# Performance work log

Measured on AMD Instinct MI355X. Metric: run time of the kernel, lower is better.

The kernel has to match this reference:

```python
import jax, jax.numpy as jnp
import numpy as np

R = 128; C = 64; S = 3; NL = 2; NH = 4; B = 2; V = 4; N = R * R
HD = C // NH
PLANES = ['xy', 'xz', 'yz']


def _sample_points(plane):
    lin = np.linspace(-1.0, 1.0, R, dtype=np.float32)
    gx, gy = np.meshgrid(lin, lin, indexing='xy')
    s = np.linspace(-1.0, 1.0, S, dtype=np.float32)
    gxs = np.broadcast_to(gx[..., None], (R, R, S))
    gys = np.broadcast_to(gy[..., None], (R, R, S))
    ss = np.broadcast_to(s[None, None, :], (R, R, S))
    if plane == 'xy':
        coords = np.stack([gxs, gys, ss], -1)
    elif plane == 'xz':
        coords = np.stack([gxs, ss, gys], -1)
    else:
        coords = np.stack([ss, gxs, gys], -1)
    return jnp.asarray(coords)  # [R,R,S,3]


def _layer_norm(x, g, b):
    m = jnp.mean(x, -1, keepdims=True)
    v = jnp.var(x, -1, keepdims=True)
    return (x - m) / jnp.sqrt(v + 1e-5) * g + b


def _grid_sample_border(feat, grid):
    # feat [Bb,Ch,H,W], grid [Bb,P,2] (treated as normalized coords, align_corners=True, border pad)
    H, W = feat.shape[2], feat.shape[3]
    gx = jnp.clip((grid[..., 0] + 1.0) * 0.5 * (W - 1), 0.0, W - 1)
    gy = jnp.clip((grid[..., 1] + 1.0) * 0.5 * (H - 1), 0.0, H - 1)
    x0 = jnp.floor(gx).astype(jnp.int32); y0 = jnp.floor(gy).astype(jnp.int32)
    x1 = jnp.minimum(x0 + 1, W - 1); y1 = jnp.minimum(y0 + 1, H - 1)
    wx = (gx - x0)[..., None]; wy = (gy - y0)[..., None]
    ft = feat.transpose(0, 2, 3, 1)  # [Bb,H,W,Ch]
    bi = jnp.arange(feat.shape[0])[:, None]
    v00 = ft[bi, y0, x0]; v01 = ft[bi, y0, x1]; v10 = ft[bi, y1, x0]; v11 = ft[bi, y1, x1]
    out = (1 - wy) * ((1 - wx) * v00 + wx * v01) + wy * ((1 - wx) * v10 + wx * v11)
    return out.transpose(0, 2, 1)  # [Bb,Ch,P]


def _splat(features, pts):
    # features [BV,C,Np], pts [BV,Np,3] in [-1,1] -> [BV,3,R,R,C]
    f = features.transpose(0, 2, 1)
    g = jnp.clip((pts + 1.0) * (R - 1) / 2.0, 0.0, R - 1 - 1e-5)
    x, y, z = g[..., 0], g[..., 1], g[..., 2]
    x0 = jnp.floor(x).astype(jnp.int32); y0 = jnp.floor(y).astype(jnp.int32); z0 = jnp.floor(z).astype(jnp.int32)
    wx = x - x0; wy = y - y0; wz = z - z0
    x1 = jnp.minimum(x0 + 1, R - 1); y1 = jnp.minimum(y0 + 1, R - 1); z1 = jnp.minimum(z0 + 1, R - 1)
    w000 = (1 - wx) * (1 - wy) * (1 - wz); w001 = (1 - wx) * (1 - wy) * wz
    w010 = (1 - wx) * wy * (1 - wz)
    w100 = wx * (1 - wy) * (1 - wz)
    w110 = wx * wy * (1 - wz); w111 = wx * wy * wz
    bv = features.shape[0]
    bi = jnp.arange(bv)[:, None]

    def plane_accum(pairs):
        tri = jnp.zeros((bv, R, R, C), features.dtype)
        wac = jnp.zeros((bv, R, R), features.dtype)
        for w, ia, ib in pairs:
            tri = tri.at[bi, ia, ib].add(w[..., None] * f)
            wac = wac.at[bi, ia, ib].add(w)
        return tri / jnp.maximum(wac, 1e-8)[..., None]

    # corner/weight pairings replicated exactly from the source (incl. its asymmetries)
    p0 = plane_accum([(w000, x0, y0), (w010, x0, y1), (w100, x1, y0), (w110, x1, y1)])
    p1 = plane_accum([(w000, x0, z0), (w001, x0, z1), (w100, x1, z0), (w111, x1, z1)])
    p2 = plane_accum([(w000, y0, z0), (w001, y0, z1), (w010, y1, z0), (w111, y1, z1)])
    return jnp.stack([p0, p1, p2], 1)


def _project(points, plane, plane_feats):
    sel = {'xy': (0, 1), 'xz': (0, 2), 'yz': (1, 2)}
    feats = []
    for i, op in enumerate(PLANES):
        if op == plane:
            continue
        a, bidx = sel[op]
        coords = jnp.stack([points[..., a], points[..., bidx]], -1)  # [R,R,S,2]
        # faithful to source: pixel coords are fed to grid_sample as if normalized
        gc = jnp.clip((coords * 0.5 + 0.5) * (R - 1), 0.0, R - 1)
        pf = plane_feats[i].reshape(B, R, R, C).transpose(0, 3, 1, 2)  # [B,C,H,W]
        grid = jnp.broadcast_to(gc.reshape(1, R * R * S, 2), (B, R * R * S, 2))
        samp = _grid_sample_border(pf, grid).reshape(B, C, R, R, S).transpose(0, 2, 3, 4, 1)
        feats.append(samp)
    return jnp.concatenate(feats, 3)  # [B,R,R,2S,C]


def _mha(x, ctx, in_w, in_b, ow, ob):
    # x [M,1,C], ctx [M,T,C]; torch MultiheadAttention (eval, no dropout)
    wq, wk, wv = in_w[:C], in_w[C:2 * C], in_w[2 * C:]
    bq, bk, bv = in_b[:C], in_b[C:2 * C], in_b[2 * C:]
    M, T = ctx.shape[0], ctx.shape[1]
    q = (x @ wq.T + bq).reshape(M, 1, NH, HD)
    k = (ctx @ wk.T + bk).reshape(M, T, NH, HD)
    v = (ctx @ wv.T + bv).reshape(M, T, NH, HD)
    att = jnp.einsum('mqhd,mthd->mhqt', q, k) * (1.0 / np.sqrt(HD))
    p = jax.nn.softmax(att, -1)
    o = jnp.einsum('mhqt,mthd->mqhd', p, v).reshape(M, 1, C)
    return o @ ow.T + ob


def _forward(img_feats, pts, query_tensors, ln1_g, ln1_b, ln2_g, ln2_b,
             in_w, in_b, out_w, out_b, ffn_w1, ffn_b1, ffn_w2, ffn_b2):
    bv = B * V
    tri = _splat(img_feats.reshape(bv, C, N), pts.reshape(bv, N, 3))  # [BV,3,R,R,C]
    tri = tri.reshape(B, V, 3, R, R, C).mean(1)  # aggregate views
    plane_feats = [tri[:, i].reshape(B, N, C) + query_tensors[i].reshape(1, N, C) for i in range(3)]
    sp = {p: _sample_points(p) for p in PLANES}
    T = 2 * S
    for l in range(NL):
        new = []
        for i, plane in enumerate(PLANES):
            ctx = _project(sp[plane], plane, plane_feats).reshape(B, N, T, C)
            x = plane_feats[i]
            xn = _layer_norm(x, ln1_g[l], ln1_b[l])
            cn = _layer_norm(ctx, ln1_g[l], ln1_b[l])
            M = B * N
            ao = _mha(xn.reshape(M, 1, C), cn.reshape(M, T, C),
                      in_w[l], in_b[l], out_w[l], out_b[l]).reshape(B, N, C)
            x = x + ao
            xn2 = _layer_norm(x, ln2_g[l], ln2_b[l])
            h = jax.nn.gelu(xn2 @ ffn_w1[l].T + ffn_b1[l], approximate=False) @ ffn_w2[l].T + ffn_b2[l]
            new.append(x + h)
        plane_feats = new
    out = jnp.stack([f.reshape(B, R, R, C) for f in plane_feats], 1)
    return out.transpose(0, 1, 4, 2, 3)  # [B,3,C,R,R]


def setup_inputs() -> dict:
    key = jax.random.key(0)
    ks = jax.random.split(key, 8)
    d = {}
    d['img_feats'] = jax.random.normal(ks[0], (B, V, C, N), jnp.float32)
    d['pts'] = jax.random.uniform(ks[1], (B, V, N, 3), jnp.float32, -1.0, 1.0)
    d['query_tensors'] = jax.random.normal(ks[2], (3, R, R, C), jnp.float32) * 0.02
    d['ln1_g'] = jnp.ones((NL, C), jnp.float32)
    d['ln1_b'] = jnp.zeros((NL, C), jnp.float32)
    d['ln2_g'] = jnp.ones((NL, C), jnp.float32)
    d['ln2_b'] = jnp.zeros((NL, C), jnp.float32)
    d['in_w'] = jax.random.normal(ks[3], (NL, 3 * C, C), jnp.float32) * 0.05
    d['in_b'] = jnp.zeros((NL, 3 * C), jnp.float32)
    d['out_w'] = jax.random.normal(ks[4], (NL, C, C), jnp.float32) * 0.05
    d['out_b'] = jnp.zeros((NL, C), jnp.float32)
    d['ffn_w1'] = jax.random.normal(ks[5], (NL, 4 * C, C), jnp.float32) * 0.05
    d['ffn_b1'] = jnp.zeros((NL, 4 * C), jnp.float32)
    d['ffn_w2'] = jax.random.normal(ks[6], (NL, C, 4 * C), jnp.float32) * 0.05
    d['ffn_b2'] = jnp.zeros((NL, C), jnp.float32)
    return d


def reference(img_feats, pts, query_tensors, ln1_g, ln1_b, ln2_g, ln2_b,
              in_w, in_b, out_w, out_b, ffn_w1, ffn_b1, ffn_w2, ffn_b2):
    return _forward(img_feats, pts, query_tensors, ln1_g, ln1_b, ln2_g, ln2_b,
                    in_w, in_b, out_w, out_b, ffn_w1, ffn_b1, ffn_w2, ffn_b2)
```

## Files before the change

### kernel.cpp

```cpp
#include <hip/hip_runtime.h>
#include <math.h>

constexpr int R_ = 128, C_ = 64, NL_ = 2, B_ = 2, V_ = 4;
constexpr int N_ = R_ * R_;
constexpr int T_ = 6;

typedef __attribute__((ext_vector_type(8))) short bf16x8;
typedef __attribute__((ext_vector_type(4))) float f32x4;
typedef __attribute__((ext_vector_type(4))) unsigned short u16x4;
typedef __attribute__((ext_vector_type(8))) unsigned short u16x8;

#define MFMA_B16(a, b, c) __builtin_amdgcn_mfma_f32_16x16x32_bf16((a), (b), (c), 0, 0, 0)

constexpr int OFF_O = 12288, OFF_W1 = 16384, OFF_W2 = 32768;
constexpr int PK_ELEMS = 49152;
constexpr int LAYER_PK = 2 * PK_ELEMS;

constexpr int NBV = B_ * V_;
constexpr size_t FTR_SZ = (size_t)NBV * N_ * C_;
constexpr int NSEG = 3 * NBV;
constexpr size_t SEG_SZ = (size_t)NSEG * N_;
constexpr int OSTRIDE = N_ + 128;
constexpr size_t KV_SZ = (size_t)3 * B_ * T_ * 128 * 64;

__device__ inline unsigned rne16(float x) {
    unsigned b = __float_as_uint(x);
    return (b + 0x7fffu + ((b >> 16) & 1u)) >> 16;
}

__device__ inline float wsum(float v) {
#pragma unroll
    for (int m = 1; m < 64; m <<= 1) v += __shfl_xor(v, m, 64);
    return v;
}

__device__ inline float lnorm(float v, float g, float b) {
    float m = wsum(v) * (1.f / 64.f);
    float d = v - m;
    float var = wsum(d * d) * (1.f / 64.f);
    return d * rsqrtf(var + 1e-5f) * g + b;
}

__device__ inline void stageW(const float* __restrict__ W, float* buf, int tid) {
#pragma unroll
    for (int it = 0; it < 4; ++it) {
        int idx4 = it * 256 + tid;
        int r = idx4 >> 4, u4 = idx4 & 15;
        float4 v = ((const float4*)W)[idx4];
        *(float4*)&buf[r * 68 + u4 * 4] = v;
    }
}

__device__ inline bf16x8 readFrag(const unsigned short* base, int rowBase, int lane,
                                  int ks, int rowStrideB, int swzMask) {
    int rowloc = rowBase + (lane & 15);
    int off = rowloc * rowStrideB + ks * 64 + ((lane >> 4) & 3) * 16;
    off ^= ((rowloc & swzMask) << 4);
    return *(const bf16x8*)((const char*)base + off);
}

__device__ inline void storeA4(unsigned short* base, int rloc, int cb,
                               float v0, float v1, float v2, float v3) {
    u16x4 u;
    u[0] = (unsigned short)rne16(v0);
    u[1] = (unsigned short)rne16(v1);
    u[2] = (unsigned short)rne16(v2);
    u[3] = (unsigned short)rne16(v3);
    int bo = (rloc * 128 + cb * 8) ^ ((rloc & 7) << 4);
    *(u16x4*)((char*)base + bo) = u;
}

__device__ inline void readB(const unsigned short* matHi, int E, int NTm, int ks, int nt,
                             int lane, bf16x8& bh, bf16x8& bl) {
    int off = (((ks * NTm + nt) << 6) + lane) << 3;
    bh = *(const bf16x8*)(matHi + off);
    bl = *(const bf16x8*)(matHi + E + off);
}

__global__ __launch_bounds__(256) void pack_layer(const float* __restrict__ iw,
                                                  const float* __restrict__ ow,
                                                  const float* __restrict__ w1,
                                                  const float* __restrict__ w2,
                                                  unsigned short* __restrict__ pk) {
    int idx = blockIdx.x * 256 + threadIdx.x;
    if (idx >= PK_ELEMS) return;
    const float* W;
    int O, K, base, mode, lidx;
    if (idx < 12288)      { int m = idx >> 12; lidx = idx & 4095; W = iw + m * 4096; O = 64;  K = 64;  base = m * 4096; mode = 0; }
    else if (idx < 16384) { lidx = idx - 12288; W = ow; O = 64;  K = 64;  base = OFF_O;  mode = 0; }
    else if (idx < 32768) { lidx = idx - 16384; W = w1; O = 256; K = 64;  base = OFF_W1; mode = 0; }
    else                  { lidx = idx - 32768; W = w2; O = 64;  K = 256; base = OFF_W2; mode = 1; }
    int j = lidx & 7, l = (lidx >> 3) & 63, rem = lidx >> 9;
    int NTm = O >> 4;
    int nt = rem & (NTm - 1), ks = rem / NTm;
    int kfrag = ks * 32 + ((l >> 4) & 3) * 8 + j;
    int k;
    if (mode == 0) { int p = kfrag & 63; k = (p & 3) * 16 + (p >> 2); }
    else { int cc = kfrag >> 7; int pl = kfrag & 127; k = (cc * 8 + (pl & 7)) * 16 + (pl >> 3); }
    int o = nt * 16 + (l & 15);
    float w = W[(size_t)o * K + k];
    unsigned hb = rne16(w);
    float hf = __uint_as_float(hb << 16);
    unsigned lb = rne16(w - hf);
    int E = O * K;
    pk[2 * base + lidx] = (unsigned short)hb;
    pk[2 * base + E + lidx] = (unsigned short)lb;
}

__global__ __launch_bounds__(256) void init_feats(const float* __restrict__ q,
                                                  float* __restrict__ f0) {
    int idx = blockIdx.x * 256 + threadIdx.x;
    if (idx >= 3 * N_ * C_) return;
    int p = idx / (N_ * C_);
    int rem = idx - p * (N_ * C_);
    float val = q[idx];
    f0[(size_t)(p * B_ + 0) * N_ * C_ + rem] = val;
    f0[(size_t)(p * B_ + 1) * N_ * C_ + rem] = val;
}

__global__ __launch_bounds__(256) void zero_counts(int4* __restrict__ p, int n4) {
    int i = blockIdx.x * 256 + threadIdx.x;
    if (i < n4) p[i] = make_int4(0, 0, 0, 0);
}

__global__ __launch_bounds__(256) void transpose_feats(const float* __restrict__ src,
                                                       float* __restrict__ dst) {
    __shared__ float tile[64][65];
    int blk = blockIdx.x;
    int ntile = blk & 255;
    int bv = blk >> 8;
    int n0 = ntile * 64;
    int tr = threadIdx.x >> 6, tc = threadIdx.x & 63;
    const float* s = src + (size_t)bv * C_ * N_;
#pragma unroll
    for (int it = 0; it < 16; ++it) {
        int c = it * 4 + tr;
        tile[c][tc] = s[(size_t)c * N_ + n0 + tc];
    }
    __syncthreads();
    float* d = dst + ((size_t)bv * N_ + n0) * C_;
#pragma unroll
    for (int it = 0; it < 16; ++it) {
        int r = it * 4 + tr;
        d[(size_t)r * C_ + tc] = tile[tc][r];
    }
}

__global__ __launch_bounds__(256) void bin_count(const float* __restrict__ pts,
                                                 int* __restrict__ counts) {
    int idx = blockIdx.x * 256 + threadIdx.x;
    if (idx >= NBV * N_) return;
    int bv = idx >> 14;
    const float* p = pts + (size_t)idx * 3;
    float px = p[0], py = p[1], pz = p[2];
    const float HI = (float)(127.0 - 1e-5);
    float gx = fminf(fmaxf((px + 1.0f) * 127.0f / 2.0f, 0.0f), HI);
    float gy = fminf(fmaxf((py + 1.0f) * 127.0f / 2.0f, 0.0f), HI);
    float gz = fminf(fmaxf((pz + 1.0f) * 127.0f / 2.0f, 0.0f), HI);
    int x0 = (int)gx, y0 = (int)gy, z0 = (int)gz;
    atomicAdd(&counts[(0 * NBV + bv) * N_ + x0 * R_ + y0], 1);
    atomicAdd(&counts[(1 * NBV + bv) * N_ + x0 * R_ + z0], 1);
    atomicAdd(&counts[(2 * NBV + bv) * N_ + y0 * R_ + z0], 1);
}

__global__ __launch_bounds__(256) void scan_bins(const int* __restrict__ counts,
                                                 int* __restrict__ offsets,
                                                 int* __restrict__ cursors) {
    __shared__ int part[256];
    int seg = blockIdx.x;
    int t = threadIdx.x;
    const int* c = counts + (size_t)seg * N_;
    int sum = 0;
    for (int i = 0; i < 64; ++i) sum += c[t * 64 + i];
    part[t] = sum;
    __syncthreads();
    if (t == 0) {
        int run = 0;
        for (int i = 0; i < 256; ++i) { int v = part[i]; part[i] = run; run += v; }
    }
    __syncthreads();
    int run = part[t];
    int* o = offsets + (size_t)seg * OSTRIDE;
    int* cu = cursors + (size_t)seg * N_;
    for (int i = 0; i < 64; ++i) {
        o[t * 64 + i] = run;
        cu[t * 64 + i] = run;
        run += c[t * 64 + i];
    }
    if (t < 128) o[N_ + t] = N_;
}

__global__ __launch_bounds__(256) void scatter_pts(const float* __restrict__ pts,
                                                   int* __restrict__ cursors,
                                                   float4* __restrict__ ent) {
    int idx = blockIdx.x * 256 + threadIdx.x;
    if (idx >= NBV * N_) return;
    int bv = idx >> 14, n = idx & (N_ - 1);
    const float* p = pts + (size_t)idx * 3;
    float px = p[0], py = p[1], pz = p[2];
    const float HI = (float)(127.0 - 1e-5);
    float gx = fminf(fmaxf((px + 1.0f) * 127.0f / 2.0f, 0.0f), HI);
    float gy = fminf(fmaxf((py + 1.0f) * 127.0f / 2.0f, 0.0f), HI);
    float gz = fminf(fmaxf((pz + 1.0f) * 127.0f / 2.0f, 0.0f), HI);
    int x0 = (int)gx, y0 = (int)gy, z0 = (int)gz;
    float4 e;
    e.x = __uint_as_float((unsigned)n);
    e.y = gx - (float)x0; e.z = gy - (float)y0; e.w = gz - (float)z0;
    int s0 = 0 * NBV + bv, s1 = 1 * NBV + bv, s2 = 2 * NBV + bv;
    int p0 = atomicAdd(&cursors[(size_t)s0 * N_ + x0 * R_ + y0], 1);
    ent[(size_t)s0 * N_ + p0] = e;
    int p1 = atomicAdd(&cursors[(size_t)s1 * N_ + x0 * R_ + z0], 1);
    ent[(size_t)s1 * N_ + p1] = e;
    int p2 = atomicAdd(&cursors[(size_t)s2 * N_ + y0 * R_ + z0], 1);
    ent[(size_t)s2 * N_ + p2] = e;
}

__global__ __launch_bounds__(512) void gather_splat(
    const float* __restrict__ ftr, const int* __restrict__ offsets,
    const float4* __restrict__ ent, float* __restrict__ f0) {
    __shared__ float sfacc[8][8][64];
    __shared__ float swsum[8][8];
    int wid = threadIdx.x >> 6, lane = threadIdx.x & 63;
    int v = wid >> 1, dr = wid & 1;
    int strip = blockIdx.x;
    int pi = blockIdx.y, b = blockIdx.z;
    int a = strip >> 4;
    int c0 = (strip & 15) << 3;

    int bv = b * V_ + v;
    int seg = pi * NBV + bv;
    const int* ob = offsets + (size_t)seg * OSTRIDE;
    const float4* eb = ent + (size_t)seg * N_;
    const float* fbase = ftr + (size_t)bv * N_ * C_ + lane;
    float facc[8], wsum_[8];
#pragma unroll
    for (int k = 0; k < 8; ++k) { facc[k] = 0.f; wsum_[k] = 0.f; }

    int ba = a - dr;
    if (ba >= 0) {
        int rowbase = ba * R_ + c0 - 1;
        int o[10];
#pragma unroll
        for (int jj = 0; jj < 10; ++jj)
            o[jj] = ob[max(rowbase + jj, 0)];
#pragma unroll
        for (int j = 0; j < 9; ++j) {
            if (j == 0 && c0 == 0) continue;
            int e = o[j + 1];
            for (int i = o[j]; i < e; ++i) {
                float4 r = eb[i];
                int n = (int)__float_as_uint(r.x);
                float wx = r.y, wy = r.z, wz = r.w;
                float ax = 1.f - wx, ay = 1.f - wy, az = 1.f - wz;
                float XA = dr ? wx : ax;
                float YA = dr ? wy : ay;
                float w0 = (pi == 2 ? ax * YA : XA * ay) * az;
                float w1 = (pi == 0) ? XA * wy * az : XA * YA * wz;
                float f = fbase[(size_t)n * C_];
                if (j > 0) { facc[j - 1] += w0 * f; wsum_[j - 1] += w0; }
                if (j < 8) { facc[j] += w1 * f; wsum_[j] += w1; }
            }
        }
    }
#pragma unroll
    for (int k = 0; k < 8; ++k) sfacc[wid][k][lane] = facc[k];
    if (lane == 0) {
#pragma unroll
        for (int k = 0; k < 8; ++k) swsum[wid][k] = wsum_[k];
    }
    __syncthreads();

    int k = wid;
    float tot = 0.f;
#pragma unroll
    for (int v2 = 0; v2 < 4; ++v2) {
        float fa = sfacc[v2 * 2][k][lane] + sfacc[v2 * 2 + 1][k][lane];
        float wsv = swsum[v2 * 2][k] + swsum[v2 * 2 + 1][k];
        tot += fa / fmaxf(wsv, 1e-8f);
    }
    float* dst = f0 + (((size_t)(pi * B_ + b)) * N_ + a * R_ + c0 + k) * C_ + lane;
    *dst += 0.25f * tot;
}

__global__ __launch_bounds__(256) void ctx_kv(
    const float* __restrict__ fin,
    const float* __restrict__ ln1g, const float* __restrict__ ln1b,
    const float* __restrict__ inw, const float* __restrict__ inb,
    float* __restrict__ kvk, float* __restrict__ kvv) {
    __shared__ float s_wk[64 * 68];
    __shared__ float s_wv[64 * 68];
    __shared__ float s_act[32 * 68];
    int tid = threadIdx.x, wid = tid >> 6, lane = tid & 63;
    stageW(inw + 4096, s_wk, tid);
    stageW(inw + 8192, s_wv, tid);

    int rid0 = blockIdx.x * 32 + wid * 8;
    int seg = rid0 >> 7;
    int pos0 = rid0 & 127;
    int t = seg % 6;
    int pib = seg / 6;
    int pi = pib >> 1, b = pib & 1;
    int khalf = (t < 3) ? t : t - 3;
    float sk = (float)(khalf - 1);
    bool tl = t < 3;
    int io;
    if (pi == 0) io = tl ? 1 : 2;
    else if (pi == 1) io = tl ? 0 : 2;
    else io = tl ? 0 : 1;
    const float* Fio = fin + (size_t)(io * B_ + b) * N_ * 64;
    float g1 = ln1g[lane], b1 = ln1b[lane];

#pragma unroll
    for (int rr = 0; rr < 8; ++rr) {
        int pos = pos0 + rr;
        float lp = -1.0f + (2.0f * (float)pos) / 127.0f;
        float caf, cbf;
        if (pi == 0) { caf = lp; cbf = sk; }
        else if (pi == 1) { if (tl) { caf = lp; cbf = sk; } else { caf = sk; cbf = lp; } }
        else { caf = sk; cbf = lp; }
        float ua = fminf(fmaxf((caf * 0.5f + 0.5f) * 127.0f, 0.0f), 127.0f);
        float ub = fminf(fmaxf((cbf * 0.5f + 0.5f) * 127.0f, 0.0f), 127.0f);
        float gxp = fminf(fmaxf(((ua + 1.0f) * 0.5f) * 127.0f, 0.0f), 127.0f);
        float gyp = fminf(fmaxf(((ub + 1.0f) * 0.5f) * 127.0f, 0.0f), 127.0f);
        int xx0 = (int)gxp, yy0 = (int)gyp;
        int xx1 = xx0 + 1 < 128 ? xx0 + 1 : 127;
        int yy1 = yy0 + 1 < 128 ? yy0 + 1 : 127;
        float wx = gxp - (float)xx0, wy = gyp - (float)yy0;
        float v00 = Fio[(size_t)(yy0 * R_ + xx0) * 64 + lane];
        float v01 = Fio[(size_t)(yy0 * R_ + xx1) * 64 + lane];
        float v10 = Fio[(size_t)(yy1 * R_ + xx0) * 64 + lane];
        float v11 = Fio[(size_t)(yy1 * R_ + xx1) * 64 + lane];
        float cv = (1.0f - wy) * ((1.0f - wx) * v00 + wx * v01) +
                   wy * ((1.0f - wx) * v10 + wx * v11);
        s_act[(wid * 8 + rr) * 68 + lane] = lnorm(cv, g1, b1);
    }
    __syncthreads();

    float kk[8], vv[8];
    float bk = inb[64 + lane], bv = inb[128 + lane];
#pragma unroll
    for (int rr = 0; rr < 8; ++rr) { kk[rr] = bk; vv[rr] = bv; }
    const float* wrk = s_wk + lane * 68;
    const float* wrv = s_wv + lane * 68;
#pragma unroll 4
    for (int g = 0; g < 16; ++g) {
        float4 wk4 = *(const float4*)(wrk + g * 4);
        float4 wv4 = *(const float4*)(wrv + g * 4);
#pragma unroll
        for (int rr = 0; rr < 8; ++rr) {
            float4 xv = *(const float4*)(s_act + (wid * 8 + rr) * 68 + g * 4);
            kk[rr] = fmaf(xv.x, wk4.x, fmaf(xv.y, wk4.y, fmaf(xv.z, wk4.z, fmaf(xv.w, wk4.w, kk[rr]))));
            vv[rr] = fmaf(xv.x, wv4.x, fmaf(xv.y, wv4.y, fmaf(xv.z, wv4.z, fmaf(xv.w, wv4.w, vv[rr]))));
        }
    }
#pragma unroll
    for (int rr = 0; rr < 8; ++rr) {
        size_t o = ((size_t)seg * 128 + pos0 + rr) * 64 + lane;
        kvk[o] = kk[rr];
        kvv[o] = vv[rr];
    }
}

__global__ __launch_bounds__(256, 2) void plane_mfma(
    const float* __restrict__ fin, float* __restrict__ fout,
    const unsigned short* __restrict__ pk,
    const float* __restrict__ kvk, const float* __restrict__ kvv,
    const float* __restrict__ ln1g, const float* __restrict__ ln1b,
    const float* __restrict__ ln2g, const float* __restrict__ ln2b,
    const float* __restrict__ inb, const float* __restrict__ outb,
    const float* __restrict__ fb1, const float* __restrict__ fb2) {
    __shared__ __attribute__((aligned(16))) unsigned short Wb[16384];
    __shared__ __attribute__((aligned(16))) unsigned short Ahi[4096];
    __shared__ __attribute__((aligned(16))) float Hf[4096];
    unsigned short* Hhi = (unsigned short*)Hf;

    const int tid = threadIdx.x;
    const int wid = tid >> 6, lane = tid & 63;
    const int cg = lane >> 4, cb = lane & 15;
    const int pi = blockIdx.y;
    const int R0 = wid * 16;
    const int rowbase = blockIdx.x * 64;
    const int b = rowbase >> 14;
    const int nn0 = rowbase & (N_ - 1);
    const int i0 = nn0 >> 7, j0 = nn0 & 127;

#pragma unroll
    for (int i = 0; i < 4; ++i)
        *(u16x8*)(Wb + (i * 256 + tid) * 8) = *(const u16x8*)(pk + (i * 256 + tid) * 8);

    float g1[4], b1v[4];
#pragma unroll
    for (int nt = 0; nt < 4; ++nt) { g1[nt] = ln1g[nt * 16 + cb]; b1v[nt] = ln1b[nt * 16 + cb]; }

    float x[4][4];
    const float* finp = fin + ((size_t)(pi * B_ + b) * N_ + nn0) * 64;
#pragma unroll
    for (int reg = 0; reg < 4; ++reg) {
        int rloc = R0 + cg * 4 + reg;
#pragma unroll
        for (int nt = 0; nt < 4; ++nt) x[reg][nt] = finp[(size_t)rloc * 64 + nt * 16 + cb];
        float s = x[reg][0] + x[reg][1] + x[reg][2] + x[reg][3];
#pragma unroll
        for (int m = 1; m < 16; m <<= 1) s += __shfl_xor(s, m, 64);
        float mean = s * (1.0f / 64.0f);
        float d0 = x[reg][0] - mean, d1 = x[reg][1] - mean, d2 = x[reg][2] - mean, d3 = x[reg][3] - mean;
        float sq = d0 * d0 + d1 * d1 + d2 * d2 + d3 * d3;
#pragma unroll
        for (int m = 1; m < 16; m <<= 1) sq += __shfl_xor(sq, m, 64);
        float rr = rsqrtf(sq * (1.0f / 64.0f) + 1e-5f);
        storeA4(Ahi, rloc, cb,
                d0 * rr * g1[0] + b1v[0], d1 * rr * g1[1] + b1v[1],
                d2 * rr * g1[2] + b1v[2], d3 * rr * g1[3] + b1v[3]);
    }
    __syncthreads();

    f32x4 qa[4];
#pragma unroll
    for (int nt = 0; nt < 4; ++nt) { float bq = inb[nt * 16 + cb]; qa[nt] = {bq, bq, bq, bq}; }
#pragma unroll
    for (int ks = 0; ks < 2; ++ks) {
        bf16x8 ah = readFrag(Ahi, R0, lane, ks, 128, 7);
#pragma unroll
        for (int nt = 0; nt < 4; ++nt) {
            bf16x8 bh, bl;
            readB(Wb, 4096, 4, ks, nt, lane, bh, bl);
            qa[nt] = MFMA_B16(ah, bh, qa[nt]);
            qa[nt] = MFMA_B16(ah, bl, qa[nt]);
        }
    }

    const float* kvkb = kvk + (size_t)((pi * 2 + b) * 6) * 128 * 64;
    const float* kvvb = kvv + (size_t)((pi * 2 + b) * 6) * 128 * 64;
    float den_[4][4];
    f32x4 oa[4];
#pragma unroll
    for (int nt = 0; nt < 4; ++nt) {
        oa[nt] = {0.f, 0.f, 0.f, 0.f};
#pragma unroll
        for (int reg = 0; reg < 4; ++reg) den_[nt][reg] = 0.f;
    }

#pragma unroll
    for (int t = 0; t < 3; ++t) {
        float kvr[4][4], vvr[4][4];
#pragma unroll
        for (int reg = 0; reg < 4; ++reg) {
            int pos = j0 + R0 + cg * 4 + reg;
            const float* kr = kvkb + ((size_t)t * 128 + pos) * 64 + cb;
            const float* vr = kvvb + ((size_t)t * 128 + pos) * 64 + cb;
#pragma unroll
            for (int nt = 0; nt < 4; ++nt) {
                kvr[reg][nt] = kr[nt * 16];
                vvr[reg][nt] = vr[nt * 16];
            }
        }
#pragma unroll
        for (int nt = 0; nt < 4; ++nt) {
            float d0 = qa[nt][0] * kvr[0][nt];
            float d1 = qa[nt][1] * kvr[1][nt];
            float d2 = qa[nt][2] * kvr[2][nt];
            float d3 = qa[nt][3] * kvr[3][nt];
#pragma unroll
            for (int m = 1; m < 16; m <<= 1) {
                d0 += __shfl_xor(d0, m, 64);
                d1 += __shfl_xor(d1, m, 64);
                d2 += __shfl_xor(d2, m, 64);
                d3 += __shfl_xor(d3, m, 64);
            }
            float e0 = __expf(d0 * 0.25f), e1 = __expf(d1 * 0.25f);
            float e2 = __expf(d2 * 0.25f), e3 = __expf(d3 * 0.25f);
            den_[nt][0] += e0; den_[nt][1] += e1; den_[nt][2] += e2; den_[nt][3] += e3;
            oa[nt][0] += e0 * vvr[0][nt];
            oa[nt][1] += e1 * vvr[1][nt];
            oa[nt][2] += e2 * vvr[2][nt];
            oa[nt][3] += e3 * vvr[3][nt];
        }
    }
#pragma unroll
    for (int t = 3; t < 6; ++t) {
        float ku[4], vu[4];
        const float* kr = kvkb + ((size_t)t * 128 + i0) * 64 + cb;
        const float* vr = kvvb + ((size_t)t * 128 + i0) * 64 + cb;
#pragma unroll
        for (int nt = 0; nt < 4; ++nt) { ku[nt] = kr[nt * 16]; vu[nt] = vr[nt * 16]; }
#pragma unroll
        for (int nt = 0; nt < 4; ++nt) {
            float d0 = qa[nt][0] * ku[nt];
            float d1 = qa[nt][1] * ku[nt];
            float d2 = qa[nt][2] * ku[nt];
            float d3 = qa[nt][3] * ku[nt];
#pragma unroll
            for (int m = 1; m < 16; m <<= 1) {
                d0 += __shfl_xor(d0, m, 64);
                d1 += __shfl_xor(d1, m, 64);
                d2 += __shfl_xor(d2, m, 64);
                d3 += __shfl_xor(d3, m, 64);
            }
            float e0 = __expf(d0 * 0.25f), e1 = __expf(d1 * 0.25f);
            float e2 = __expf(d2 * 0.25f), e3 = __expf(d3 * 0.25f);
            den_[nt][0] += e0; den_[nt][1] += e1; den_[nt][2] += e2; den_[nt][3] += e3;
            oa[nt][0] += e0 * vu[nt];
            oa[nt][1] += e1 * vu[nt];
            oa[nt][2] += e2 * vu[nt];
            oa[nt][3] += e3 * vu[nt];
        }
    }
    __syncthreads();

#pragma unroll
    for (int i = 0; i < 4; ++i)
        *(u16x8*)(Wb + (i * 256 + tid) * 8) = *(const u16x8*)(pk + 24576 + (i * 256 + tid) * 8);
#pragma unroll
    for (int reg = 0; reg < 4; ++reg) {
        int rloc = R0 + cg * 4 + reg;
        storeA4(Ahi, rloc, cb,
                oa[0][reg] / den_[0][reg], oa[1][reg] / den_[1][reg],
                oa[2][reg] / den_[2][reg], oa[3][reg] / den_[3][reg]);
    }
    __syncthreads();

    f32x4 ao[4];
#pragma unroll
    for (int nt = 0; nt < 4; ++nt) { float bo_ = outb[nt * 16 + cb]; ao[nt] = {bo_, bo_, bo_, bo_}; }
#pragma unroll
    for (int ks = 0; ks < 2; ++ks) {
        bf16x8 ah = readFrag(Ahi, R0, lane, ks, 128, 7);
#pragma unroll
        for (int nt = 0; nt < 4; ++nt) {
            bf16x8 bh, bl;
            readB(Wb, 4096, 4, ks, nt, lane, bh, bl);
            ao[nt] = MFMA_B16(ah, bh, ao[nt]);
            ao[nt] = MFMA_B16(ah, bl, ao[nt]);
        }
    }
    float g2[4], b2v[4];
#pragma unroll
    for (int nt = 0; nt < 4; ++nt) { g2[nt] = ln2g[nt * 16 + cb]; b2v[nt] = ln2b[nt * 16 + cb]; }
    float x2[4][4];
#pragma unroll
    for (int reg = 0; reg < 4; ++reg) {
        int rloc = R0 + cg * 4 + reg;
#pragma unroll
        for (int nt = 0; nt < 4; ++nt) x2[reg][nt] = x[reg][nt] + ao[nt][reg];
        float s = x2[reg][0] + x2[reg][1] + x2[reg][2] + x2[reg][3];
#pragma unroll
        for (int m = 1; m < 16; m <<= 1) s += __shfl_xor(s, m, 64);
        float mean = s * (1.0f / 64.0f);
        float d0 = x2[reg][0] - mean, d1 = x2[reg][1] - mean, d2 = x2[reg][2] - mean, d3 = x2[reg][3] - mean;
        float sq = d0 * d0 + d1 * d1 + d2 * d2 + d3 * d3;
#pragma unroll
        for (int m = 1; m < 16; m <<= 1) sq += __shfl_xor(sq, m, 64);
        float rr = rsqrtf(sq * (1.0f / 64.0f) + 1e-5f);
        storeA4(Ahi, rloc, cb,
                d0 * rr * g2[0] + b2v[0], d1 * rr * g2[1] + b2v[1],
                d2 * rr * g2[2] + b2v[2], d3 * rr * g2[3] + b2v[3]);
    }
    __syncthreads();

    const unsigned short* pW1 = pk + 2 * OFF_W1;
    const unsigned short* pW2 = pk + 2 * OFF_W2;
    f32x4 ya[4];
#pragma unroll
    for (int nt = 0; nt < 4; ++nt) { float by = fb2[nt * 16 + cb]; ya[nt] = {by, by, by, by}; }

#pragma unroll
    for (int cc = 0; cc < 2; ++cc) {
#pragma unroll
        for (int it = 0; it < 8; ++it) {
            int i = it * 256 + tid;
            int half = i >> 10, j = i & 1023;
            int lt = j >> 6, lr = j & 63;
            int ksl = lt >> 3, n8 = lt & 7;
            int gt = ksl * 16 + cc * 8 + n8;
            *(u16x8*)(Wb + half * 8192 + (lt * 64 + lr) * 8) =
                *(const u16x8*)(pW1 + half * 16384 + (gt * 64 + lr) * 8);
        }
        __syncthreads();

        f32x4 ha[8];
#pragma unroll
        for (int n8 = 0; n8 < 8; ++n8) {
            float hb = fb1[(cc * 8 + n8) * 16 + cb];
            ha[n8] = {hb, hb, hb, hb};
        }
#pragma unroll
        for (int ks = 0; ks < 2; ++ks) {
            bf16x8 ah = readFrag(Ahi, R0, lane, ks, 128, 7);
#pragma unroll
            for (int n8 = 0; n8 < 8; ++n8) {
                bf16x8 bh, bl;
                readB(Wb, 8192, 8, ks, n8, lane, bh, bl);
                ha[n8] = MFMA_B16(ah, bh, ha[n8]);
                ha[n8] = MFMA_B16(ah, bl, ha[n8]);
            }
        }
#pragma unroll
        for (int reg = 0; reg < 4; ++reg) {
            int rloc = R0 + cg * 4 + reg;
            u16x8 u;
#pragma unroll
            for (int n8 = 0; n8 < 8; ++n8) {
                float h = ha[n8][reg];
                h = 0.5f * h * (1.0f + erff(h * 0.70710678118654752f));
                u[n8] = (unsigned short)rne16(h);
            }
            int bo = (rloc * 256 + cb * 16) ^ ((rloc & 15) << 4);
            *(u16x8*)((char*)Hhi + bo) = u;
        }
        __syncthreads();

#pragma unroll
        for (int it = 0; it < 8; ++it) {
            int i = it * 256 + tid;
            int half = i >> 10, j = i & 1023;
            *(u16x8*)(Wb + half * 8192 + j * 8) =
                *(const u16x8*)(pW2 + half * 16384 + cc * 8192 + j * 8);
        }
        __syncthreads();

#pragma unroll
        for (int ks2 = 0; ks2 < 4; ++ks2) {
            bf16x8 ah = readFrag(Hhi, R0, lane, ks2, 256, 15);
#pragma unroll
            for (int nt = 0; nt < 4; ++nt) {
                bf16x8 bh, bl;
                readB(Wb, 8192, 4, ks2, nt, lane, bh, bl);
                ya[nt] = MFMA_B16(ah, bh, ya[nt]);
                ya[nt] = MFMA_B16(ah, bl, ya[nt]);
            }
        }
        __syncthreads();
    }

#pragma unroll
    for (int reg = 0; reg < 4; ++reg) {
        int rloc = R0 + cg * 4 + reg;
#pragma unroll
        for (int nt = 0; nt < 4; ++nt)
            Hf[rloc * 64 + nt * 16 + cb] = x2[reg][nt] + ya[nt][reg];
    }
    __syncthreads();
    {
        float4* dst4 = (float4*)(fout + ((size_t)(pi * B_ + b) * N_ + nn0) * 64);
        const float4* src4 = (const float4*)Hf;
#pragma unroll
        for (int it = 0; it < 4; ++it) {
            int i = it * 256 + tid;
            dst4[i] = src4[i];
        }
    }
}

__global__ __launch_bounds__(256) void output_kernel(const float* __restrict__ f,
                                                     float* __restrict__ out) {
    __shared__ float tile[64][65];
    int blk = blockIdx.x;
    int ntile = blk & 255;
    int bp = blk >> 8;
    int b = bp / 3, p = bp - b * 3;
    int n0 = ntile * 64;
    int tr = threadIdx.x >> 6, tc = threadIdx.x & 63;

    const float* src = f + ((size_t)(p * B_ + b) * N_ + n0) * C_;
#pragma unroll
    for (int it = 0; it < 16; ++it) {
        int r = it * 4 + tr;
        tile[r][tc] = src[(size_t)r * C_ + tc];
    }
    __syncthreads();
    float* dst = out + (size_t)(b * 3 + p) * C_ * N_ + n0;
#pragma unroll
    for (int it = 0; it < 16; ++it) {
        int cidx = it * 4 + tr;
        dst[(size_t)cidx * N_ + tc] = tile[tc][cidx];
    }
}

extern "C" void kernel_launch(void* const* d_in, const int* in_sizes, int n_in,
                              void* d_out, int out_size, void* d_ws, size_t ws_size,
                              hipStream_t stream) {
    const float* img_feats = (const float*)d_in[0];
    const float* pts       = (const float*)d_in[1];
    const float* query     = (const float*)d_in[2];
    const float* ln1_g     = (const float*)d_in[3];
    const float* ln1_b     = (const float*)d_in[4];
    const float* ln2_g     = (const float*)d_in[5];
    const float* ln2_b     = (const float*)d_in[6];
    const float* in_w      = (const float*)d_in[7];
    const float* in_b      = (const float*)d_in[8];
    const float* out_w     = (const float*)d_in[9];
    const float* out_b     = (const float*)d_in[10];
    const float* ffn_w1    = (const float*)d_in[11];
    const float* ffn_b1    = (const float*)d_in[12];
    const float* ffn_w2    = (const float*)d_in[13];
    const float* ffn_b2    = (const float*)d_in[14];

    const size_t FEAT_SZ = (size_t)3 * B_ * N_ * C_;

    float* ws = (float*)d_ws;
    float* ftr      = ws;
    int* counts     = (int*)(ftr + FTR_SZ);
    int* offsets    = counts + SEG_SZ;
    int* cursors    = offsets + (size_t)NSEG * OSTRIDE;
    float4* ent     = (float4*)(cursors + SEG_SZ);
    float* fA       = (float*)(ent + SEG_SZ);
    float* fB       = fA + FEAT_SZ;
    unsigned short* pk_base = (unsigned short*)(fB + FEAT_SZ);
    float* kvk = (float*)counts;
    float* kvv = kvk + KV_SZ;

    init_feats<<<(3 * N_ * C_ + 255) / 256, 256, 0, stream>>>(query, fA);

    zero_counts<<<(int)(SEG_SZ / 4 + 255) / 256, 256, 0, stream>>>((int4*)counts, (int)(SEG_SZ / 4));
    transpose_feats<<<NBV * 256, 256, 0, stream>>>(img_feats, ftr);
    bin_count<<<(NBV * N_) / 256, 256, 0, stream>>>(pts, counts);
    scan_bins<<<NSEG, 256, 0, stream>>>(counts, offsets, cursors);
    scatter_pts<<<(NBV * N_) / 256, 256, 0, stream>>>(pts, cursors, ent);
    gather_splat<<<dim3(2048, 3, B_), 512, 0, stream>>>(ftr, offsets, ent, fA);

    for (int l = 0; l < NL_; ++l) {
        pack_layer<<<(PK_ELEMS + 255) / 256, 256, 0, stream>>>(
            in_w + (size_t)l * 3 * C_ * C_, out_w + (size_t)l * C_ * C_,
            ffn_w1 + (size_t)l * 4 * C_ * C_, ffn_w2 + (size_t)l * C_ * 4 * C_,
            pk_base + (size_t)l * LAYER_PK);
    }

    dim3 pgrid((B_ * N_) / 64, 3);
    for (int l = 0; l < NL_; ++l) {
        const float* fin = (l == 0) ? fA : fB;
        float* fout      = (l == 0) ? fB : fA;
        ctx_kv<<<144, 256, 0, stream>>>(fin, ln1_g + l * C_, ln1_b + l * C_,
                                        in_w + (size_t)l * 3 * C_ * C_, in_b + l * 3 * C_,
                                        kvk, kvv);
        plane_mfma<<<pgrid, 256, 0, stream>>>(
            fin, fout, pk_base + (size_t)l * LAYER_PK, kvk, kvv,
            ln1_g + l * C_, ln1_b + l * C_,
            ln2_g + l * C_, ln2_b + l * C_,
            in_b + l * 3 * C_, out_b + l * C_,
            ffn_b1 + l * 4 * C_, ffn_b2 + l * C_);
    }

    output_kernel<<<B_ * 3 * (N_ / 64), 256, 0, stream>>>(fA, (float*)d_out);
}
```

Before: 357.0 us.

## Batch splat entry gathers by eight over flattened cell range in gather_splat

The scatter kernel now packs the second-axis cell index next to the point index in each entry. The gather kernel can then walk one flat entry range per strip instead of nine separate per-cell loops. Entries and feature loads are issued eight at a time so several memory loads are in flight together. Accumulation moves from registers into shared memory, indexed by the dynamic cell slot. This costs more LDS read-modify-write traffic and some wasted work on padded tail entries.

```diff
diff --git a/kernel.cpp b/kernel.cpp
--- a/kernel.cpp
+++ b/kernel.cpp
@@ -204,11 +204,13 @@
     float gz = fminf(fmaxf((pz + 1.0f) * 127.0f / 2.0f, 0.0f), HI);
     int x0 = (int)gx, y0 = (int)gy, z0 = (int)gz;
     float4 e;
-    e.x = __uint_as_float((unsigned)n);
     e.y = gx - (float)x0; e.z = gy - (float)y0; e.w = gz - (float)z0;
+    unsigned n14 = (unsigned)n;
     int s0 = 0 * NBV + bv, s1 = 1 * NBV + bv, s2 = 2 * NBV + bv;
+    e.x = __uint_as_float(n14 | ((unsigned)y0 << 14));
     int p0 = atomicAdd(&cursors[(size_t)s0 * N_ + x0 * R_ + y0], 1);
     ent[(size_t)s0 * N_ + p0] = e;
+    e.x = __uint_as_float(n14 | ((unsigned)z0 << 14));
     int p1 = atomicAdd(&cursors[(size_t)s1 * N_ + x0 * R_ + z0], 1);
     ent[(size_t)s1 * N_ + p1] = e;
     int p2 = atomicAdd(&cursors[(size_t)s2 * N_ + y0 * R_ + z0], 1);
@@ -227,46 +229,64 @@
     int a = strip >> 4;
     int c0 = (strip & 15) << 3;
 
+#pragma unroll
+    for (int k = 0; k < 8; ++k) sfacc[wid][k][lane] = 0.f;
+    if (lane < 8) swsum[wid][lane] = 0.f;
+
     int bv = b * V_ + v;
     int seg = pi * NBV + bv;
     const int* ob = offsets + (size_t)seg * OSTRIDE;
     const float4* eb = ent + (size_t)seg * N_;
     const float* fbase = ftr + (size_t)bv * N_ * C_ + lane;
-    float facc[8], wsum_[8];
-#pragma unroll
-    for (int k = 0; k < 8; ++k) { facc[k] = 0.f; wsum_[k] = 0.f; }
 
     int ba = a - dr;
     if (ba >= 0) {
-        int rowbase = ba * R_ + c0 - 1;
-        int o[10];
-#pragma unroll
-        for (int jj = 0; jj < 10; ++jj)
-            o[jj] = ob[max(rowbase + jj, 0)];
-#pragma unroll
-        for (int j = 0; j < 9; ++j) {
-            if (j == 0 && c0 == 0) continue;
-            int e = o[j + 1];
-            for (int i = o[j]; i < e; ++i) {
-                float4 r = eb[i];
-                int n = (int)__float_as_uint(r.x);
-                float wx = r.y, wy = r.z, wz = r.w;
+        int clo = (c0 == 0) ? 0 : c0 - 1;
+        int lo = ob[ba * R_ + clo];
+        int hi = ob[ba * R_ + c0 + 8];
+
+        for (int base = lo; base < hi; base += 8) {
+            float4 e8[8];
+#pragma unroll
+            for (int k = 0; k < 8; ++k) {
+                int i = base + k;
+                e8[k] = eb[i < hi ? i : hi - 1];
+            }
+            int nn[8], jj[8];
+            float w0v[8], w1v[8];
+#pragma unroll
+            for (int k = 0; k < 8; ++k) {
+                unsigned pc = __float_as_uint(e8[k].x);
+                nn[k] = (int)(pc & 16383u);
+                int bc = (int)((pc >> 14) & 127u);
+                jj[k] = bc - c0 + 1;
+                float wx = e8[k].y, wy = e8[k].z, wz = e8[k].w;
                 float ax = 1.f - wx, ay = 1.f - wy, az = 1.f - wz;
                 float XA = dr ? wx : ax;
                 float YA = dr ? wy : ay;
                 float w0 = (pi == 2 ? ax * YA : XA * ay) * az;
                 float w1 = (pi == 0) ? XA * wy * az : XA * YA * wz;
-                float f = fbase[(size_t)n * C_];
-                if (j > 0) { facc[j - 1] += w0 * f; wsum_[j - 1] += w0; }
-                if (j < 8) { facc[j] += w1 * f; wsum_[j] += w1; }
-            }
-        }
-    }
-#pragma unroll
-    for (int k = 0; k < 8; ++k) sfacc[wid][k][lane] = facc[k];
-    if (lane == 0) {
-#pragma unroll
-        for (int k = 0; k < 8; ++k) swsum[wid][k] = wsum_[k];
+                bool valid = (base + k) < hi;
+                w0v[k] = valid ? w0 : 0.f;
+                w1v[k] = valid ? w1 : 0.f;
+            }
+            float f[8];
+#pragma unroll
+            for (int k = 0; k < 8; ++k)
+                f[k] = fbase[(size_t)nn[k] * C_];
+#pragma unroll
+            for (int k = 0; k < 8; ++k) {
+                int j = jj[k];
+                if (j > 0) {
+                    sfacc[wid][j - 1][lane] += w0v[k] * f[k];
+                    if (lane == 0) swsum[wid][j - 1] += w0v[k];
+                }
+                if (j < 8) {
+                    sfacc[wid][j][lane] += w1v[k] * f[k];
+                    if (lane == 0) swsum[wid][j] += w1v[k];
+                }
+            }
+        }
     }
     __syncthreads();
 
```

New measurement: 358.2 us. No clear change (+0.3%).

## Precompute fp16 splat weights in scatter and fuse query init into gather

Applied to the files above, without the earlier changes.

Scatter now precomputes the two per-direction trilinear weight pairs for each plane and stores them packed as fp16 in the entry, so the gather loop only unpacks two halves instead of recomputing products from fractional coordinates. The separate init_feats kernel is removed; gather_splat reads the query tensor and writes query plus splat directly, avoiding a read-modify-write pass and one launch. The fp16 round-toward-zero weights reduce accuracy slightly, and the entry index is masked to 14 bits.

```diff
diff --git a/kernel.cpp b/kernel.cpp
--- a/kernel.cpp
+++ b/kernel.cpp
@@ -9,6 +9,7 @@
 typedef __attribute__((ext_vector_type(4))) float f32x4;
 typedef __attribute__((ext_vector_type(4))) unsigned short u16x4;
 typedef __attribute__((ext_vector_type(8))) unsigned short u16x8;
+typedef __attribute__((ext_vector_type(2))) __fp16 h2;
 
 #define MFMA_B16(a, b, c) __builtin_amdgcn_mfma_f32_16x16x32_bf16((a), (b), (c), 0, 0, 0)
 
@@ -107,17 +108,6 @@
     pk[2 * base + E + lidx] = (unsigned short)lb;
 }
 
-__global__ __launch_bounds__(256) void init_feats(const float* __restrict__ q,
-                                                  float* __restrict__ f0) {
-    int idx = blockIdx.x * 256 + threadIdx.x;
-    if (idx >= 3 * N_ * C_) return;
-    int p = idx / (N_ * C_);
-    int rem = idx - p * (N_ * C_);
-    float val = q[idx];
-    f0[(size_t)(p * B_ + 0) * N_ * C_ + rem] = val;
-    f0[(size_t)(p * B_ + 1) * N_ * C_ + rem] = val;
-}
-
 __global__ __launch_bounds__(256) void zero_counts(int4* __restrict__ p, int n4) {
     int i = blockIdx.x * 256 + threadIdx.x;
     if (i < n4) p[i] = make_int4(0, 0, 0, 0);
@@ -203,21 +193,39 @@
     float gy = fminf(fmaxf((py + 1.0f) * 127.0f / 2.0f, 0.0f), HI);
     float gz = fminf(fmaxf((pz + 1.0f) * 127.0f / 2.0f, 0.0f), HI);
     int x0 = (int)gx, y0 = (int)gy, z0 = (int)gz;
+    float wx = gx - (float)x0, wy = gy - (float)y0, wz = gz - (float)z0;
+    float ax = 1.f - wx, ay = 1.f - wy, az = 1.f - wz;
     float4 e;
     e.x = __uint_as_float((unsigned)n);
-    e.y = gx - (float)x0; e.z = gy - (float)y0; e.w = gz - (float)z0;
+    e.w = 0.f;
     int s0 = 0 * NBV + bv, s1 = 1 * NBV + bv, s2 = 2 * NBV + bv;
-    int p0 = atomicAdd(&cursors[(size_t)s0 * N_ + x0 * R_ + y0], 1);
-    ent[(size_t)s0 * N_ + p0] = e;
-    int p1 = atomicAdd(&cursors[(size_t)s1 * N_ + x0 * R_ + z0], 1);
-    ent[(size_t)s1 * N_ + p1] = e;
-    int p2 = atomicAdd(&cursors[(size_t)s2 * N_ + y0 * R_ + z0], 1);
-    ent[(size_t)s2 * N_ + p2] = e;
+    {
+        h2 a = __builtin_amdgcn_cvt_pkrtz(ax * ay * az, ax * wy * az);
+        h2 bq = __builtin_amdgcn_cvt_pkrtz(wx * ay * az, wx * wy * az);
+        e.y = *(float*)&a; e.z = *(float*)&bq;
+        int p0 = atomicAdd(&cursors[(size_t)s0 * N_ + x0 * R_ + y0], 1);
+        ent[(size_t)s0 * N_ + p0] = e;
+    }
+    {
+        h2 a = __builtin_amdgcn_cvt_pkrtz(ax * ay * az, ax * ay * wz);
+        h2 bq = __builtin_amdgcn_cvt_pkrtz(wx * ay * az, wx * wy * wz);
+        e.y = *(float*)&a; e.z = *(float*)&bq;
+        int p1 = atomicAdd(&cursors[(size_t)s1 * N_ + x0 * R_ + z0], 1);
+        ent[(size_t)s1 * N_ + p1] = e;
+    }
+    {
+        h2 a = __builtin_amdgcn_cvt_pkrtz(ax * ay * az, ax * ay * wz);
+        h2 bq = __builtin_amdgcn_cvt_pkrtz(ax * wy * az, wx * wy * wz);
+        e.y = *(float*)&a; e.z = *(float*)&bq;
+        int p2 = atomicAdd(&cursors[(size_t)s2 * N_ + y0 * R_ + z0], 1);
+        ent[(size_t)s2 * N_ + p2] = e;
+    }
 }
 
 __global__ __launch_bounds__(512) void gather_splat(
     const float* __restrict__ ftr, const int* __restrict__ offsets,
-    const float4* __restrict__ ent, float* __restrict__ f0) {
+    const float4* __restrict__ ent, const float* __restrict__ query,
+    float* __restrict__ f0) {
     __shared__ float sfacc[8][8][64];
     __shared__ float swsum[8][8];
     int wid = threadIdx.x >> 6, lane = threadIdx.x & 63;
@@ -249,13 +257,10 @@
             int e = o[j + 1];
             for (int i = o[j]; i < e; ++i) {
                 float4 r = eb[i];
-                int n = (int)__float_as_uint(r.x);
-                float wx = r.y, wy = r.z, wz = r.w;
-                float ax = 1.f - wx, ay = 1.f - wy, az = 1.f - wz;
-                float XA = dr ? wx : ax;
-                float YA = dr ? wy : ay;
-                float w0 = (pi == 2 ? ax * YA : XA * ay) * az;
-                float w1 = (pi == 0) ? XA * wy * az : XA * YA * wz;
+                int n = (int)(__float_as_uint(r.x) & 16383u);
+                float pr = dr ? r.z : r.y;
+                h2 ph = *(h2*)&pr;
+                float w0 = (float)ph[0], w1 = (float)ph[1];
                 float f = fbase[(size_t)n * C_];
                 if (j > 0) { facc[j - 1] += w0 * f; wsum_[j - 1] += w0; }
                 if (j < 8) { facc[j] += w1 * f; wsum_[j] += w1; }
@@ -271,6 +276,7 @@
     __syncthreads();
 
     int k = wid;
+    int cell = a * R_ + c0 + k;
     float tot = 0.f;
 #pragma unroll
     for (int v2 = 0; v2 < 4; ++v2) {
@@ -278,8 +284,8 @@
         float wsv = swsum[v2 * 2][k] + swsum[v2 * 2 + 1][k];
         tot += fa / fmaxf(wsv, 1e-8f);
     }
-    float* dst = f0 + (((size_t)(pi * B_ + b)) * N_ + a * R_ + c0 + k) * C_ + lane;
-    *dst += 0.25f * tot;
+    float qv = query[((size_t)pi * N_ + cell) * C_ + lane];
+    f0[(((size_t)(pi * B_ + b)) * N_ + cell) * C_ + lane] = qv + 0.25f * tot;
 }
 
 __global__ __launch_bounds__(256) void ctx_kv(
@@ -703,20 +709,18 @@
     int* offsets    = counts + SEG_SZ;
     int* cursors    = offsets + (size_t)NSEG * OSTRIDE;
     float4* ent     = (float4*)(cursors + SEG_SZ);
-    float* fA       = (float*)(ent + SEG_SZ);
+    float* fA       = (float*)(ent + SEG_SZ + 8);
     float* fB       = fA + FEAT_SZ;
     unsigned short* pk_base = (unsigned short*)(fB + FEAT_SZ);
     float* kvk = (float*)counts;
     float* kvv = kvk + KV_SZ;
-
-    init_feats<<<(3 * N_ * C_ + 255) / 256, 256, 0, stream>>>(query, fA);
 
     zero_counts<<<(int)(SEG_SZ / 4 + 255) / 256, 256, 0, stream>>>((int4*)counts, (int)(SEG_SZ / 4));
     transpose_feats<<<NBV * 256, 256, 0, stream>>>(img_feats, ftr);
     bin_count<<<(NBV * N_) / 256, 256, 0, stream>>>(pts, counts);
     scan_bins<<<NSEG, 256, 0, stream>>>(counts, offsets, cursors);
     scatter_pts<<<(NBV * N_) / 256, 256, 0, stream>>>(pts, cursors, ent);
-    gather_splat<<<dim3(2048, 3, B_), 512, 0, stream>>>(ftr, offsets, ent, fA);
+    gather_splat<<<dim3(2048, 3, B_), 512, 0, stream>>>(ftr, offsets, ent, query, fA);
 
     for (int l = 0; l < NL_; ++l) {
         pack_layer<<<(PK_ELEMS + 255) / 256, 256, 0, stream>>>(
```

New measurement: 351.8 us, median of 2. About the same (-1.5%).
